# Kernel tuning notes

Measured on AMD Instinct MI355X. Metric: run time of the kernel, lower is better.

## Reference

```python
import jax, jax.numpy as jnp
import numpy as np

N = 50000
E = 1600000
IN_C = 32
OUT_C = 32
OUT_SIZE = 1


def setup_inputs() -> dict:
    key = jax.random.key(0)
    ks = jax.random.split(key, 16)
    x = jax.random.normal(ks[0], (N, IN_C), dtype=jnp.float32)
    edge_index = jax.random.randint(ks[1], (2, E), 0, N, dtype=jnp.int64)

    def glorot(k, shape):
        lim = float(np.sqrt(6.0 / (shape[0] + shape[1])))
        return jax.random.uniform(k, shape, jnp.float32, -lim, lim)

    params = {
        # GCNConv weights for gates z, r, h: [in, out] and bias [out]
        'Wz_c': glorot(ks[2], (IN_C, OUT_C)), 'bz_c': jnp.zeros((OUT_C,), jnp.float32),
        'Wr_c': glorot(ks[3], (IN_C, OUT_C)), 'br_c': jnp.zeros((OUT_C,), jnp.float32),
        'Wh_c': glorot(ks[4], (IN_C, OUT_C)), 'bh_c': jnp.zeros((OUT_C,), jnp.float32),
        # GRU linear layers: [2*out, out] and bias [out]
        'Wz_l': glorot(ks[5], (2 * OUT_C, OUT_C)), 'bz_l': jnp.zeros((OUT_C,), jnp.float32),
        'Wr_l': glorot(ks[6], (2 * OUT_C, OUT_C)), 'br_l': jnp.zeros((OUT_C,), jnp.float32),
        'Wh_l': glorot(ks[7], (2 * OUT_C, OUT_C)), 'bh_l': jnp.zeros((OUT_C,), jnp.float32),
        # final readout Linear(out_channels, output_size)
        'W_lin': glorot(ks[8], (OUT_C, OUT_SIZE)), 'b_lin': jnp.zeros((OUT_SIZE,), jnp.float32),
    }
    return {'x': x, 'edge_index': edge_index, **params}


def _gcn_conv(x, W, b, src, dst, n_nodes):
    """GCNConv with add_self_loops=False, symmetric normalization."""
    h = x @ W  # [N, out]
    ones = jnp.ones((src.shape[0],), h.dtype)
    deg = jax.ops.segment_sum(ones, dst, num_segments=n_nodes)  # in-degree at targets
    dinv = jnp.where(deg > 0, jax.lax.rsqrt(jnp.maximum(deg, 1e-12)), 0.0)
    norm = dinv[src] * dinv[dst]  # [E]
    msg = h[src] * norm[:, None]  # gather + scale
    agg = jax.ops.segment_sum(msg, dst, num_segments=n_nodes)  # scatter-add
    return agg + b


def reference(x, edge_index, Wz_c, bz_c, Wr_c, br_c, Wh_c, bh_c,
              Wz_l, bz_l, Wr_l, br_l, Wh_l, bh_l, W_lin, b_lin):
    src, dst = edge_index[0], edge_index[1]
    n = x.shape[0]
    H = jnp.zeros((n, OUT_C), x.dtype)  # H=None -> zeros

    Z = jax.nn.sigmoid(jnp.concatenate([_gcn_conv(x, Wz_c, bz_c, src, dst, n), H], axis=1) @ Wz_l + bz_l)
    R = jax.nn.sigmoid(jnp.concatenate([_gcn_conv(x, Wr_c, br_c, src, dst, n), H], axis=1) @ Wr_l + br_l)
    H_tilde = jnp.tanh(jnp.concatenate([_gcn_conv(x, Wh_c, bh_c, src, dst, n), H * R], axis=1) @ Wh_l + bh_l)
    H = Z * H + (1.0 - Z) * H_tilde

    h = jax.nn.relu(H)
    return h @ W_lin + b_lin  # [N, output_size]
```

## Files before the change

### kernel.cpp

```cpp
#include <hip/hip_runtime.h>
#include <hip/hip_fp16.h>
#include <math.h>

#define NN 50000
#define NE 1600000
#define ELLW 80
#define SHN 6250
#define XH_WORDS 800016

#define NBIN 400
#define BINW 125
#define NBLK 782
#define HDRW 404
#define MAGIC125 34359739u

#define NEED_A ((4000000ull + 800000 + 800000 + 50000 + 2112) * 4)
#define NEED_B ((4000000ull + 800000 + 50000 + 2112) * 4)

struct h2x2 { __half2 a, b; };

__global__ __launch_bounds__(512) void bucket_kernel(
        const int* __restrict__ ei,
        unsigned int* __restrict__ bkt, unsigned int* __restrict__ hdr,
        const float* __restrict__ Wz_c, const float* __restrict__ bz_c,
        const float* __restrict__ Wh_c, const float* __restrict__ bh_c,
        const float* __restrict__ Wz_l, const float* __restrict__ bz_l,
        const float* __restrict__ Wh_l, const float* __restrict__ bh_l,
        float* __restrict__ Mz, float* __restrict__ Mh,
        float* __restrict__ cz, float* __restrict__ ch,
        __half2* __restrict__ xh) {
    int t = threadIdx.x;
    int b = blockIdx.x;
    if (b >= NBLK) {
        for (int p = t; p < 1024; p += 512) {
            int i = p >> 5, j = p & 31;
            float az = 0.0f, ah = 0.0f;
            for (int k = 0; k < 32; ++k) {
                az += Wz_c[i * 32 + k] * Wz_l[k * 32 + j];
                ah += Wh_c[i * 32 + k] * Wh_l[k * 32 + j];
            }
            Mz[p] = az;
            Mh[p] = ah;
        }
        if (t < 32) {
            int j = t;
            float sz = bz_l[j], sh = bh_l[j];
            for (int k = 0; k < 32; ++k) {
                sz += bz_c[k] * Wz_l[k * 32 + j];
                sh += bh_c[k] * Wh_l[k * 32 + j];
            }
            cz[j] = sz;
            ch[j] = sh;
        }
        if (xh && t < 16) ((unsigned int*)xh)[NN * 16 + t] = 0u;
        return;
    }
    __shared__ unsigned int lcnt[NBIN];
    __shared__ unsigned int lstart[NBIN];
    __shared__ unsigned int loff[NBIN];
    __shared__ unsigned int wtot[8];
    __shared__ alignas(16) unsigned int stage[2048];
    for (int i = t; i < NBIN; i += 512) lcnt[i] = 0u;
    __syncthreads();
    int i4 = b * 512 + t;
    bool valid = (i4 < NE / 4);
    int4 s4 = make_int4(0, 0, 0, 0), d4 = make_int4(0, 0, 0, 0);
    if (valid) {
        s4 = ((const int4*)ei)[i4];
        d4 = ((const int4*)(ei + NE))[i4];
#define CNT_E(dd, ss)                                                       \
        if ((unsigned)(dd) < NN && (unsigned)(ss) < NN)                     \
            atomicAdd(&lcnt[__umulhi((unsigned)(dd), MAGIC125)], 1u);
        CNT_E(d4.x, s4.x) CNT_E(d4.y, s4.y) CNT_E(d4.z, s4.z) CNT_E(d4.w, s4.w)
#undef CNT_E
    }
    __syncthreads();
    unsigned xval = (t < NBIN) ? lcnt[t] : 0u;
    unsigned sc = xval;
    #pragma unroll
    for (int off = 1; off < 64; off <<= 1) {
        unsigned v = __shfl_up(sc, off);
        if ((t & 63) >= off) sc += v;
    }
    if ((t & 63) == 63) wtot[t >> 6] = sc;
    __syncthreads();
    unsigned wpre = 0;
    for (int ww = 0; ww < (t >> 6); ++ww) wpre += wtot[ww];
    sc += wpre;
    if (t < NBIN) {
        unsigned st = sc - xval;
        lstart[t] = st;
        loff[t] = st;
        hdr[b * HDRW + t] = st;
    }
    if (t == NBIN - 1) hdr[b * HDRW + NBIN] = sc;
    __syncthreads();
    if (valid) {
#define SC_E(dd, ss)                                                        \
        if ((unsigned)(dd) < NN && (unsigned)(ss) < NN) {                   \
            unsigned bn = __umulhi((unsigned)(dd), MAGIC125);               \
            unsigned p = atomicAdd(&loff[bn], 1u);                          \
            stage[p] = ((unsigned)(dd) << 16) | (unsigned)(ss);             \
        }
        SC_E(d4.x, s4.x) SC_E(d4.y, s4.y) SC_E(d4.z, s4.z) SC_E(d4.w, s4.w)
#undef SC_E
    }
    __syncthreads();
    ((uint4*)bkt)[b * 512 + t] = ((const uint4*)stage)[t];
}

__global__ __launch_bounds__(512) void build_ell_kernel(const unsigned int* __restrict__ bkt,
                                                        const unsigned int* __restrict__ hdr,
                                                        unsigned int* __restrict__ cnt,
                                                        float* __restrict__ dinv,
                                                        unsigned short* __restrict__ ell,
                                                        const float* __restrict__ x,
                                                        __half2* __restrict__ xh) {
    __shared__ unsigned int lcnt[BINW];
    __shared__ float ldinv[BINW];
    __shared__ alignas(16) unsigned short stage[BINW * ELLW];
    int t = threadIdx.x;
    int blk = blockIdx.x;
    int bin = (blk & 7) * 50 + (blk >> 3);
    int nbase = bin * BINW;
    for (int i = t; i < BINW; i += 512) lcnt[i] = 0u;
    __syncthreads();
    for (int b = t; b < NBLK; b += 512) {
        unsigned o0 = hdr[b * HDRW + bin];
        unsigned o1 = hdr[b * HDRW + bin + 1];
        const unsigned int* bp = bkt + b * 2048;
        for (unsigned i = o0; i < o1; ++i) {
            unsigned v = bp[i];
            unsigned ld = (v >> 16) - (unsigned)nbase;
            unsigned p = atomicAdd(&lcnt[ld], 1u);
            if (p < ELLW) stage[ld * ELLW + p] = (unsigned short)(v & 0xffffu);
        }
    }
    __syncthreads();
    const uint2* st2 = (const uint2*)stage;
    uint2* ell2 = (uint2*)(ell + (size_t)nbase * ELLW);
    for (int p = t; p < BINW * 20; p += 512) {
        int i = p / 20, c = p % 20;
        if ((unsigned)(c * 4) < lcnt[i]) ell2[p] = st2[p];
    }
    for (int i = t; i < BINW; i += 512) {
        unsigned d = lcnt[i];
        float dv = d ? rsqrtf((float)d) : 0.0f;
        cnt[nbase + i] = d;
        dinv[nbase + i] = dv;
        ldinv[i] = dv;
    }
    if (xh) {
        __syncthreads();
        const float2* x2 = (const float2*)x;
        for (int p = t; p < BINW * 16; p += 512) {
            int i = p >> 4, c = p & 15;
            float2 v = x2[(size_t)(nbase + i) * 16 + c];
            float dv = ldinv[i];
            xh[(size_t)(nbase + i) * 16 + c] = __floats2half2_rn(v.x * dv, v.y * dv);
        }
    }
}

template <int USE_H>
__global__ __launch_bounds__(256) void gather_node_kernel(const unsigned short* __restrict__ ell,
                                                          const unsigned int* __restrict__ cnt,
                                                          const float* __restrict__ dinv,
                                                          const float* __restrict__ x,
                                                          const h2x2* __restrict__ xh,
                                                          const float* __restrict__ Mz,
                                                          const float* __restrict__ Mh,
                                                          const float* __restrict__ cz,
                                                          const float* __restrict__ ch,
                                                          const float* __restrict__ Wlin,
                                                          const float* __restrict__ blin,
                                                          float* __restrict__ out) {
    __shared__ float sMz[1024], sMh[1024], scz[32], sch[32], sw[32];
    __shared__ float xs[8][32];
    int t = threadIdx.x;
    for (int i = t; i < 1024; i += 256) { sMz[i] = Mz[i]; sMh[i] = Mh[i]; }
    if (t < 32) { scz[t] = cz[t]; sch[t] = ch[t]; sw[t] = Wlin[t]; }
    __syncthreads();

    int l    = t & 63;
    int slot = t >> 5;
    int q    = l & 31;
    int hb   = l & 32;
    int shard = blockIdx.x & 7;
    int grp   = blockIdx.x >> 3;
    int ns = grp * 8 + slot;
    if (ns >= SHN) return;
    int n = shard * SHN + ns;

    int base = n * ELLW;
    int len0 = (int)cnt[n];
    float dn = len0 ? rsqrtf((float)len0) : 0.0f;
    int len = len0 > ELLW ? ELLW : len0;
    int lenW = max(len, __shfl_xor(len, 32));

    const float4* x4 = (const float4*)x;
    int es = q >> 3;
    int k  = q & 7;
    float4 acc = make_float4(0.f, 0.f, 0.f, 0.f);

    for (int c0 = 0; c0 < lenW; c0 += 32) {
        int m = len - c0; if (m > 32) m = 32;
        int mw = lenW - c0; if (mw > 32) mw = 32;
        int s; float wgt = 0.0f;
        if (USE_H) {
            s = (q < m) ? (int)ell[base + c0 + q] : NN;
        } else {
            s = 0;
            if (q < m) { s = (int)ell[base + c0 + q]; wgt = dinv[s]; }
        }
#define SW(j0) { int sl = hb + (j0) + es; int sj = __shfl(s, sl);                          \
                 if (USE_H) {                                                              \
                     h2x2 hv = xh[sj * 8 + k];                                             \
                     float2 f0 = __half22float2(hv.a), f1 = __half22float2(hv.b);          \
                     acc.x += f0.x; acc.y += f0.y;                                         \
                     acc.z += f1.x; acc.w += f1.y;                                         \
                 } else {                                                                  \
                     float wj = __shfl(wgt, sl);                                           \
                     float4 v = x4[sj * 8 + k];                                            \
                     acc.x += v.x * wj; acc.y += v.y * wj;                                 \
                     acc.z += v.z * wj; acc.w += v.w * wj;                                 \
                 } }
        SW(0) SW(4)
        if (mw > 8)  { SW(8)  SW(12) }
        if (mw > 16) { SW(16) SW(20) }
        if (mw > 24) { SW(24) SW(28) }
#undef SW
    }
    #pragma unroll
    for (int mm = 8; mm <= 16; mm <<= 1) {
        acc.x += __shfl_xor(acc.x, mm);
        acc.y += __shfl_xor(acc.y, mm);
        acc.z += __shfl_xor(acc.z, mm);
        acc.w += __shfl_xor(acc.w, mm);
    }
    if (es == 0) {
        float4* xs4 = (float4*)&xs[slot][0];
        xs4[k] = make_float4(acc.x * dn, acc.y * dn, acc.z * dn, acc.w * dn);
    }

    int j = q;
    float az = scz[j];
    float ah = sch[j];
    #pragma unroll
    for (int i = 0; i < 32; ++i) {
        float v = xs[slot][i];
        az += v * sMz[i * 32 + j];
        ah += v * sMh[i * 32 + j];
    }
    float z  = 1.0f / (1.0f + __expf(-az));
    float ht = tanhf(ah);
    float hv = (1.0f - z) * ht;
    hv = hv > 0.0f ? hv : 0.0f;
    float val = hv * sw[j];
    val += __shfl_xor(val, 1);
    val += __shfl_xor(val, 2);
    val += __shfl_xor(val, 4);
    val += __shfl_xor(val, 8);
    val += __shfl_xor(val, 16);
    if (q == 0) out[n] = val + blin[0];
}

extern "C" void kernel_launch(void* const* d_in, const int* in_sizes, int n_in,
                              void* d_out, int out_size, void* d_ws, size_t ws_size,
                              hipStream_t stream) {
    const float* x    = (const float*)d_in[0];
    const int*   ei   = (const int*)d_in[1];
    const float* Wz_c = (const float*)d_in[2];
    const float* bz_c = (const float*)d_in[3];
    const float* Wh_c = (const float*)d_in[6];
    const float* bh_c = (const float*)d_in[7];
    const float* Wz_l = (const float*)d_in[8];
    const float* bz_l = (const float*)d_in[9];
    const float* Wh_l = (const float*)d_in[12];
    const float* bh_l = (const float*)d_in[13];
    const float* Wlin = (const float*)d_in[14];
    const float* blin = (const float*)d_in[15];
    float* out = (float*)d_out;
    float* ws = (float*)d_ws;

    int use_h = (ws_size >= NEED_A) ? 1 : 0;

    unsigned short* ell16 = (unsigned short*)(ws);
    unsigned int*   cnt   = (unsigned int*)(ws + 2000000);
    __half2*        xh    = use_h ? (__half2*)(ws + 2050000) : nullptr;
    float*          dinv  = ws + 2050000 + (use_h ? XH_WORDS : 0);
    float*          Mz    = dinv + NN;
    float*          Mh    = Mz + 1024;
    float*          cz    = Mh + 1024;
    float*          ch    = cz + 32;
    unsigned int*   bkt   = (unsigned int*)(ch + 32);
    unsigned int*   hdr   = bkt + (size_t)NBLK * 2048;

    const int k1_grid    = NBLK + 1;
    const int build_grid = NBIN;
    const int node_grid  = 8 * ((SHN + 7) / 8);

    bucket_kernel<<<k1_grid, 512, 0, stream>>>(ei, bkt, hdr,
                                               Wz_c, bz_c, Wh_c, bh_c,
                                               Wz_l, bz_l, Wh_l, bh_l,
                                               Mz, Mh, cz, ch, xh);
    build_ell_kernel<<<build_grid, 512, 0, stream>>>(bkt, hdr, cnt, dinv, ell16, x, xh);
    if (use_h) {
        gather_node_kernel<1><<<node_grid, 256, 0, stream>>>(
            ell16, cnt, dinv, x, (const h2x2*)xh, Mz, Mh, cz, ch, Wlin, blin, out);
    } else {
        gather_node_kernel<0><<<node_grid, 256, 0, stream>>>(
            ell16, cnt, dinv, x, (const h2x2*)nullptr, Mz, Mh, cz, ch, Wlin, blin, out);
    }
}
```

Measured before the change: 143.2 us.

## Double edges per bucket block and transpose bin header for coalesced reads

Each bucket block now processes 2048 edges instead of 1024, halving the number of blocks and per-block header segments. The header is stored transposed (bin-major), so in the ELL build kernel each thread, one per source block, reads its offsets contiguously. With 391 blocks, every build thread handles at most one block segment instead of looping. The cost is a larger shared staging buffer (16KB), which may reduce occupancy, and more serial work per bucket block.

```diff
diff --git a/kernel.cpp b/kernel.cpp
--- a/kernel.cpp
+++ b/kernel.cpp
@@ -10,8 +10,7 @@
 
 #define NBIN 400
 #define BINW 125
-#define NBLK 782
-#define HDRW 404
+#define NBLK 391
 #define MAGIC125 34359739u
 
 #define NEED_A ((4000000ull + 800000 + 800000 + 50000 + 2112) * 4)
@@ -21,7 +20,7 @@
 
 __global__ __launch_bounds__(512) void bucket_kernel(
         const int* __restrict__ ei,
-        unsigned int* __restrict__ bkt, unsigned int* __restrict__ hdr,
+        unsigned int* __restrict__ bkt, unsigned int* __restrict__ hdrT,
         const float* __restrict__ Wz_c, const float* __restrict__ bz_c,
         const float* __restrict__ Wh_c, const float* __restrict__ bh_c,
         const float* __restrict__ Wz_l, const float* __restrict__ bz_l,
@@ -59,21 +58,22 @@
     __shared__ unsigned int lstart[NBIN];
     __shared__ unsigned int loff[NBIN];
     __shared__ unsigned int wtot[8];
-    __shared__ alignas(16) unsigned int stage[2048];
+    __shared__ alignas(16) unsigned int stage[4096];
     for (int i = t; i < NBIN; i += 512) lcnt[i] = 0u;
     __syncthreads();
-    int i4 = b * 512 + t;
-    bool valid = (i4 < NE / 4);
-    int4 s4 = make_int4(0, 0, 0, 0), d4 = make_int4(0, 0, 0, 0);
-    if (valid) {
-        s4 = ((const int4*)ei)[i4];
-        d4 = ((const int4*)(ei + NE))[i4];
+    int i40 = b * 1024 + t;
+    int i41 = i40 + 512;
+    bool v0 = (i40 < NE / 4), v1 = (i41 < NE / 4);
+    int4 sa = make_int4(0,0,0,0), da = make_int4(0,0,0,0);
+    int4 sb = make_int4(0,0,0,0), db = make_int4(0,0,0,0);
+    if (v0) { sa = ((const int4*)ei)[i40]; da = ((const int4*)(ei + NE))[i40]; }
+    if (v1) { sb = ((const int4*)ei)[i41]; db = ((const int4*)(ei + NE))[i41]; }
 #define CNT_E(dd, ss)                                                       \
-        if ((unsigned)(dd) < NN && (unsigned)(ss) < NN)                     \
-            atomicAdd(&lcnt[__umulhi((unsigned)(dd), MAGIC125)], 1u);
-        CNT_E(d4.x, s4.x) CNT_E(d4.y, s4.y) CNT_E(d4.z, s4.z) CNT_E(d4.w, s4.w)
+    if ((unsigned)(dd) < NN && (unsigned)(ss) < NN)                         \
+        atomicAdd(&lcnt[__umulhi((unsigned)(dd), MAGIC125)], 1u);
+    if (v0) { CNT_E(da.x, sa.x) CNT_E(da.y, sa.y) CNT_E(da.z, sa.z) CNT_E(da.w, sa.w) }
+    if (v1) { CNT_E(db.x, sb.x) CNT_E(db.y, sb.y) CNT_E(db.z, sb.z) CNT_E(db.w, sb.w) }
 #undef CNT_E
-    }
     __syncthreads();
     unsigned xval = (t < NBIN) ? lcnt[t] : 0u;
     unsigned sc = xval;
@@ -91,26 +91,26 @@
         unsigned st = sc - xval;
         lstart[t] = st;
         loff[t] = st;
-        hdr[b * HDRW + t] = st;
-    }
-    if (t == NBIN - 1) hdr[b * HDRW + NBIN] = sc;
-    __syncthreads();
-    if (valid) {
+        hdrT[t * NBLK + b] = st;
+    }
+    if (t == NBIN - 1) hdrT[NBIN * NBLK + b] = sc;
+    __syncthreads();
 #define SC_E(dd, ss)                                                        \
-        if ((unsigned)(dd) < NN && (unsigned)(ss) < NN) {                   \
-            unsigned bn = __umulhi((unsigned)(dd), MAGIC125);               \
-            unsigned p = atomicAdd(&loff[bn], 1u);                          \
-            stage[p] = ((unsigned)(dd) << 16) | (unsigned)(ss);             \
-        }
-        SC_E(d4.x, s4.x) SC_E(d4.y, s4.y) SC_E(d4.z, s4.z) SC_E(d4.w, s4.w)
+    if ((unsigned)(dd) < NN && (unsigned)(ss) < NN) {                       \
+        unsigned bn = __umulhi((unsigned)(dd), MAGIC125);                   \
+        unsigned p = atomicAdd(&loff[bn], 1u);                              \
+        stage[p] = ((unsigned)(dd) << 16) | (unsigned)(ss);                 \
+    }
+    if (v0) { SC_E(da.x, sa.x) SC_E(da.y, sa.y) SC_E(da.z, sa.z) SC_E(da.w, sa.w) }
+    if (v1) { SC_E(db.x, sb.x) SC_E(db.y, sb.y) SC_E(db.z, sb.z) SC_E(db.w, sb.w) }
 #undef SC_E
-    }
-    __syncthreads();
-    ((uint4*)bkt)[b * 512 + t] = ((const uint4*)stage)[t];
+    __syncthreads();
+    ((uint4*)bkt)[b * 1024 + t]       = ((const uint4*)stage)[t];
+    ((uint4*)bkt)[b * 1024 + 512 + t] = ((const uint4*)stage)[512 + t];
 }
 
 __global__ __launch_bounds__(512) void build_ell_kernel(const unsigned int* __restrict__ bkt,
-                                                        const unsigned int* __restrict__ hdr,
+                                                        const unsigned int* __restrict__ hdrT,
                                                         unsigned int* __restrict__ cnt,
                                                         float* __restrict__ dinv,
                                                         unsigned short* __restrict__ ell,
@@ -125,10 +125,10 @@
     int nbase = bin * BINW;
     for (int i = t; i < BINW; i += 512) lcnt[i] = 0u;
     __syncthreads();
-    for (int b = t; b < NBLK; b += 512) {
-        unsigned o0 = hdr[b * HDRW + bin];
-        unsigned o1 = hdr[b * HDRW + bin + 1];
-        const unsigned int* bp = bkt + b * 2048;
+    if (t < NBLK) {
+        unsigned o0 = hdrT[bin * NBLK + t];
+        unsigned o1 = hdrT[(bin + 1) * NBLK + t];
+        const unsigned int* bp = bkt + t * 4096;
         for (unsigned i = o0; i < o1; ++i) {
             unsigned v = bp[i];
             unsigned ld = (v >> 16) - (unsigned)nbase;
@@ -294,17 +294,17 @@
     float*          cz    = Mh + 1024;
     float*          ch    = cz + 32;
     unsigned int*   bkt   = (unsigned int*)(ch + 32);
-    unsigned int*   hdr   = bkt + (size_t)NBLK * 2048;
+    unsigned int*   hdrT  = bkt + (size_t)NBLK * 4096;
 
     const int k1_grid    = NBLK + 1;
     const int build_grid = NBIN;
     const int node_grid  = 8 * ((SHN + 7) / 8);
 
-    bucket_kernel<<<k1_grid, 512, 0, stream>>>(ei, bkt, hdr,
+    bucket_kernel<<<k1_grid, 512, 0, stream>>>(ei, bkt, hdrT,
                                                Wz_c, bz_c, Wh_c, bh_c,
                                                Wz_l, bz_l, Wh_l, bh_l,
                                                Mz, Mh, cz, ch, xh);
-    build_ell_kernel<<<build_grid, 512, 0, stream>>>(bkt, hdr, cnt, dinv, ell16, x, xh);
+    build_ell_kernel<<<build_grid, 512, 0, stream>>>(bkt, hdrT, cnt, dinv, ell16, x, xh);
     if (use_h) {
         gather_node_kernel<1><<<node_grid, 256, 0, stream>>>(
             ell16, cnt, dinv, x, (const h2x2*)xh, Mz, Mh, cz, ch, Wlin, blin, out);
```

Measured after the change: 140.6 us. No clear change (-1.8%).
